# Performance work log

Hardware: AMD Instinct MI355X
Metric: run time of the kernel (lower is better)

The kernel has to match this reference:

```python
import jax, jax.numpy as jnp
import numpy as np

S = 8192          # sequence length
E = 1024          # embedding_dim
H = 2048          # hidden_dim
V = 50257         # vocab_size
T = 50            # tagset_size


def setup_inputs() -> dict:
    key = jax.random.key(0)
    ks = jax.random.split(key, 5)
    scale = 0.02
    return {
        "sentence": jax.random.randint(ks[0], (S,), 0, V),
        "emb": jax.random.normal(ks[1], (V, E), jnp.float32) * scale,
        "W_ih": jax.random.normal(ks[2], (H, E), jnp.float32) * scale,
        "W_hh": jax.random.normal(ks[3], (H, H), jnp.float32) * scale,
        "b_ih": jnp.zeros((H,), jnp.float32),
        "b_hh": jnp.zeros((H,), jnp.float32),
        "W_out": jax.random.normal(ks[4], (T, H), jnp.float32) * scale,
        "b_out": jnp.zeros((T,), jnp.float32),
        "h0": jnp.zeros((H,), jnp.float32),
    }


def reference(sentence, emb, W_ih, W_hh, b_ih, b_hh, W_out, b_out, h0):
    # Embedding lookup: [S, E]
    x = emb[sentence]
    # Precompute input contribution for all timesteps (parallel GEMM): [S, H]
    xi = x @ W_ih.T + b_ih + b_hh

    # Elman recurrence: h_t = tanh(W_ih x_t + b_ih + W_hh h_{t-1} + b_hh)
    def step(h, xi_t):
        h_new = jnp.tanh(xi_t + W_hh @ h)
        return h_new, h_new

    _, rnn_out = jax.lax.scan(step, h0, xi)  # rnn_out: [S, H]

    # Linear head + log_softmax over tags
    tag_space = rnn_out @ W_out.T + b_out    # [S, T]
    return jax.nn.log_softmax(tag_space, axis=-1)
```

## Files before the change

kernel.cpp:

```cpp
#include <hip/hip_runtime.h>
#include <hip/hip_bf16.h>

#define S_LEN 8192
#define E_DIM 1024
#define H_DIM 2048
#define T_TAGS 50
#define NWG 256
#define RPW (H_DIM / NWG)

typedef short short8 __attribute__((ext_vector_type(8)));
typedef float floatx4 __attribute__((ext_vector_type(4)));
typedef _Float16 half8 __attribute__((ext_vector_type(8)));
typedef _Float16 half2v __attribute__((ext_vector_type(2)));
typedef unsigned int uint4a __attribute__((ext_vector_type(4)));

__device__ __forceinline__ unsigned short f2bf(float f) {
    unsigned u = __builtin_bit_cast(unsigned, f);
    unsigned r = (u + 0x7fffu + ((u >> 16) & 1u)) >> 16;
    return (unsigned short)r;
}

__device__ __forceinline__ float dot8(half8 a, half8 b, float acc) {
#if __has_builtin(__builtin_amdgcn_fdot2)
    union U { half8 v; half2v p[4]; };
    U ua; ua.v = a; U ub; ub.v = b;
    acc = __builtin_amdgcn_fdot2(ua.p[0], ub.p[0], acc, false);
    acc = __builtin_amdgcn_fdot2(ua.p[1], ub.p[1], acc, false);
    acc = __builtin_amdgcn_fdot2(ua.p[2], ub.p[2], acc, false);
    acc = __builtin_amdgcn_fdot2(ua.p[3], ub.p[3], acc, false);
#else
    #pragma unroll
    for (int i = 0; i < 8; ++i) acc += (float)a[i] * (float)b[i];
#endif
    return acc;
}

__device__ __forceinline__ float fast_tanh(float x) {
    float xc = fminf(fmaxf(x, -9.f), 9.f);
    float e = __expf(2.f * xc);
    return (e - 1.f) / (e + 1.f);
}

#define TAGOK(A, B)                                                          \
    (((A.x >> 16) == tg) & ((A.y >> 16) == tg) & ((A.z >> 16) == tg) &       \
     ((A.w >> 16) == tg) & ((B.x >> 16) == tg) & ((B.y >> 16) == tg) &       \
     ((B.z >> 16) == tg) & ((B.w >> 16) == tg))

__global__ __launch_bounds__(256) void cast_kernel(
        const float* __restrict__ whh, const float* __restrict__ wih,
        const float* __restrict__ wout,
        _Float16* __restrict__ whh_h, unsigned short* __restrict__ wih_b,
        _Float16* __restrict__ wout_h) {
    const int nWhh = H_DIM * H_DIM;
    const int nWih = H_DIM * E_DIM;
    const int nWout = 64 * H_DIM;
    long long i = (long long)blockIdx.x * 256 + threadIdx.x;
    if (i < nWhh) { whh_h[i] = (_Float16)whh[i]; return; }
    i -= nWhh;
    if (i < nWih) { wih_b[i] = f2bf(wih[i]); return; }
    i -= nWih;
    if (i < nWout) {
        int r = (int)(i >> 11), c = (int)(i & 2047);
        wout_h[i] = (r < T_TAGS) ? (_Float16)wout[r * H_DIM + c] : (_Float16)0.f;
    }
}

__global__ __launch_bounds__(256) void embed_kernel(
        const int* __restrict__ sent, const float* __restrict__ emb,
        unsigned short* __restrict__ Xb) {
    size_t i = (size_t)blockIdx.x * 256 + threadIdx.x;
    size_t s = i >> 10, e = i & 1023;
    Xb[i] = f2bf(emb[(size_t)sent[s] * E_DIM + e]);
}

__global__ __launch_bounds__(256) void xi_gemm(
        const unsigned short* __restrict__ Xb, const unsigned short* __restrict__ Wb,
        const float* __restrict__ bih, const float* __restrict__ bhh,
        float* __restrict__ xi) {
    int lane = threadIdx.x & 63;
    int w = threadIdx.x >> 6;
    int m0 = blockIdx.y * 64 + w * 16;
    int n0 = blockIdx.x * 16;
    int mi = m0 + (lane & 15);
    int ni = n0 + (lane & 15);
    int q8 = (lane >> 4) * 8;
    const short8* arow = (const short8*)(Xb + (size_t)mi * E_DIM + q8);
    const short8* brow = (const short8*)(Wb + (size_t)ni * E_DIM + q8);
    floatx4 acc = {0.f, 0.f, 0.f, 0.f};
    #pragma unroll 4
    for (int k = 0; k < E_DIM / 32; ++k) {
        short8 a = arow[k * 4];
        short8 b = brow[k * 4];
        acc = __builtin_amdgcn_mfma_f32_16x16x32_bf16(a, b, acc, 0, 0, 0);
    }
    float bias = bih[ni] + bhh[ni];
    int rbase = (lane >> 4) * 4;
    #pragma unroll
    for (int i = 0; i < 4; ++i) {
        xi[(size_t)(m0 + rbase + i) * H_DIM + ni] = acc[i] + bias;
    }
}

__global__ __launch_bounds__(256) void init_hpk(
        const float* __restrict__ h0, unsigned* __restrict__ hpk,
        unsigned* __restrict__ hx) {
    int i = blockIdx.x * 256 + threadIdx.x;
    if (i < H_DIM) {
        unsigned short hb = __builtin_bit_cast(unsigned short, (_Float16)h0[i]);
        unsigned pk = (unsigned)hb;
        hpk[i] = pk;
        hpk[H_DIM + i] = 0xFFFF0000u;
        #pragma unroll
        for (int x = 0; x < 8; ++x) {
            hx[(size_t)x * 2 * H_DIM + i] = pk;
            hx[(size_t)x * 2 * H_DIM + H_DIM + i] = 0xFFFF0000u;
        }
    }
}

__global__ __launch_bounds__(256, 1) void rnn_seq(
        const _Float16* __restrict__ Whh, const float* __restrict__ xi,
        unsigned* __restrict__ hpk, unsigned* __restrict__ hx,
        unsigned* __restrict__ ctl, _Float16* __restrict__ rnn) {
    __shared__ __align__(16) _Float16 hlds[2][H_DIM];
    __shared__ float xilds[2][64];
    __shared__ int sh_xcd, sh_rank, sh_fast;
    const int tid = threadIdx.x;
    const int wg = blockIdx.x;

    if (tid == 0) {
        unsigned x;
        asm volatile("s_getreg_b32 %0, hwreg(HW_REG_XCC_ID)" : "=s"(x));
        x &= 7u;
        unsigned rk = __hip_atomic_fetch_add(&ctl[x], 1u, __ATOMIC_RELAXED,
                                             __HIP_MEMORY_SCOPE_AGENT);
        __hip_atomic_fetch_add(&ctl[8], 1u, __ATOMIC_RELEASE,
                               __HIP_MEMORY_SCOPE_AGENT);
        while (__hip_atomic_load(&ctl[8], __ATOMIC_ACQUIRE,
                                 __HIP_MEMORY_SCOPE_AGENT) < (unsigned)NWG)
            __builtin_amdgcn_s_sleep(2);
        int fast = 1;
        for (int k = 0; k < 8; ++k)
            fast &= (__hip_atomic_load(&ctl[k], __ATOMIC_RELAXED,
                                       __HIP_MEMORY_SCOPE_AGENT) == 32u);
        sh_xcd = (int)x; sh_rank = (int)rk; sh_fast = fast;
    }
    __syncthreads();
    const int xcd = sh_xcd, rank = sh_rank, use_fast = sh_fast;

    if (use_fast && rank < 32) {
        const int lane = tid & 63;
        const int wv = tid >> 6;
        const int wgrow = rank * 64;
        unsigned* hxl = hx + (size_t)xcd * 2 * H_DIM;

        half8 w[16][4];
        {
            const _Float16* wb = Whh + (size_t)(wgrow + wv * 16) * H_DIM + lane * 8;
            #pragma unroll
            for (int i = 0; i < 16; ++i) {
                const half8* rp = (const half8*)(wb + (size_t)i * H_DIM);
                asm volatile(
                    "global_load_dwordx4 %0, %4, off\n\t"
                    "global_load_dwordx4 %1, %5, off\n\t"
                    "global_load_dwordx4 %2, %6, off\n\t"
                    "global_load_dwordx4 %3, %7, off\n\t"
                    "s_waitcnt vmcnt(0)"
                    : "=&v"(w[i][0]), "=&v"(w[i][1]), "=&v"(w[i][2]), "=&v"(w[i][3])
                    : "v"(rp), "v"(rp + 64), "v"(rp + 128), "v"(rp + 192));
            }
        }
        if (tid < 64) xilds[0][tid] = xi[wgrow + tid];
        __syncthreads();

        const int lr = ((lane & 1) << 3) | (((lane >> 1) & 1) << 2) |
                       (((lane >> 2) & 1) << 1) | ((lane >> 3) & 1);

        for (int t = 0; t < S_LEN; ++t) {
            float xnext = 0.f;
            if (tid < 64 && t + 1 < S_LEN)
                xnext = xi[(size_t)(t + 1) * H_DIM + wgrow + tid];

            const uint4a* p = (const uint4a*)(hxl + (size_t)(t & 1) * H_DIM) + tid * 2;
            const unsigned tg = (unsigned)t;
            uint4a a, b;
            int rounds = 0;
            for (;;) {
                if (rounds < 24) {
                    asm volatile(
                        "global_load_dwordx4 %0, %2, off sc0 nt\n\t"
                        "global_load_dwordx4 %1, %3, off sc0 nt\n\t"
                        "s_waitcnt vmcnt(0)"
                        : "=&v"(a), "=&v"(b) : "v"(p), "v"(p + 1) : "memory");
                } else {
                    asm volatile(
                        "global_load_dwordx4 %0, %2, off sc0 sc1\n\t"
                        "global_load_dwordx4 %1, %3, off sc0 sc1\n\t"
                        "s_waitcnt vmcnt(0)"
                        : "=&v"(a), "=&v"(b) : "v"(p), "v"(p + 1) : "memory");
                }
                bool ok = TAGOK(a, b);
                if (ok) break;
                ++rounds;
                if (rounds > 2) __builtin_amdgcn_s_sleep(1);
            }
            uint4a hp;
            hp.x = (a.x & 0xffffu) | (a.y << 16);
            hp.y = (a.z & 0xffffu) | (a.w << 16);
            hp.z = (b.x & 0xffffu) | (b.y << 16);
            hp.w = (b.z & 0xffffu) | (b.w << 16);
            *(uint4a*)&hlds[t & 1][tid * 8] = hp;
            if (tid < 64) xilds[(t + 1) & 1][tid] = xnext;
            __syncthreads();

            half8 hv[4];
            {
                const half8* hb = (const half8*)&hlds[t & 1][lane * 8];
                #pragma unroll
                for (int j = 0; j < 4; ++j) hv[j] = hb[j * 64];
            }
            float acc[16];
            #pragma unroll
            for (int i = 0; i < 16; ++i) {
                float s = 0.f;
                #pragma unroll
                for (int j = 0; j < 4; ++j) s = dot8(w[i][j], hv[j], s);
                acc[i] = s;
            }

            {
                bool hi = lane & 1;
                #pragma unroll
                for (int i = 0; i < 8; ++i) {
                    float snd = hi ? acc[i] : acc[i + 8];
                    float kp  = hi ? acc[i + 8] : acc[i];
                    acc[i] = kp + __shfl_xor(snd, 1);
                }
                hi = lane & 2;
                #pragma unroll
                for (int i = 0; i < 4; ++i) {
                    float snd = hi ? acc[i] : acc[i + 4];
                    float kp  = hi ? acc[i + 4] : acc[i];
                    acc[i] = kp + __shfl_xor(snd, 2);
                }
                hi = lane & 4;
                #pragma unroll
                for (int i = 0; i < 2; ++i) {
                    float snd = hi ? acc[i] : acc[i + 2];
                    float kp  = hi ? acc[i + 2] : acc[i];
                    acc[i] = kp + __shfl_xor(snd, 4);
                }
                hi = lane & 8;
                {
                    float snd = hi ? acc[0] : acc[1];
                    float kp  = hi ? acc[1] : acc[0];
                    acc[0] = kp + __shfl_xor(snd, 8);
                }
                acc[0] += __shfl_xor(acc[0], 16);
                acc[0] += __shfl_xor(acc[0], 32);
            }

            if (lane < 16) {
                int lrow = wv * 16 + lr;
                float hvf = fast_tanh(xilds[t & 1][lrow] + acc[0]);
                _Float16 hf = (_Float16)hvf;
                unsigned pk = ((unsigned)(t + 1) << 16)
                            | (unsigned)__builtin_bit_cast(unsigned short, hf);
                unsigned* dst = hxl + (size_t)((t + 1) & 1) * H_DIM + wgrow + lrow;
                asm volatile("global_store_dword %0, %1, off sc0 sc1"
                             :: "v"(dst), "v"(pk) : "memory");
                if (xcd == 0)
                    rnn[(size_t)t * H_DIM + wgrow + lrow] = hf;
            }
        }
    } else {
        const int rowbase = wg * RPW;
        const int r = tid >> 5;
        const int j = tid & 31;
        half8 wreg[8];
        {
            const half8* wrow = (const half8*)(Whh + (size_t)(rowbase + r) * H_DIM);
            #pragma unroll
            for (int c = 0; c < 8; ++c) wreg[c] = wrow[j + c * 32];
        }
        if (tid < RPW) xilds[0][tid] = xi[rowbase + tid];
        __syncthreads();

        for (int t = 0; t < S_LEN; ++t) {
            float xnext = 0.f;
            if (tid < RPW && t + 1 < S_LEN)
                xnext = xi[(size_t)(t + 1) * H_DIM + rowbase + tid];

            const uint4a* p0 = (const uint4a*)(hpk + (size_t)(t & 1) * H_DIM) + tid * 2;
            const unsigned tg = (unsigned)t;
            uint4a a = {}, b = {};
            bool got0 = false, got1 = false;
            int round = 0;
            for (;;) {
                if (!got0)
                    asm volatile("global_load_dwordx4 %0, %1, off sc0 sc1"
                                 : "=v"(a) : "v"(p0) : "memory");
                if (!got1)
                    asm volatile("global_load_dwordx4 %0, %1, off sc0 sc1"
                                 : "=v"(b) : "v"(p0 + 1) : "memory");
                asm volatile("s_waitcnt vmcnt(0)" ::: "memory");
                got0 = got0 | (((a.x >> 16) == tg) & ((a.y >> 16) == tg) &
                               ((a.z >> 16) == tg) & ((a.w >> 16) == tg));
                got1 = got1 | (((b.x >> 16) == tg) & ((b.y >> 16) == tg) &
                               ((b.z >> 16) == tg) & ((b.w >> 16) == tg));
                if (got0 && got1) break;
                if (++round > 1) __builtin_amdgcn_s_sleep(1);
            }
            uint4a hp;
            hp.x = (a.x & 0xffffu) | (a.y << 16);
            hp.y = (a.z & 0xffffu) | (a.w << 16);
            hp.z = (b.x & 0xffffu) | (b.y << 16);
            hp.w = (b.z & 0xffffu) | (b.w << 16);
            *(uint4a*)&hlds[t & 1][tid * 8] = hp;
            if (tid < RPW) xilds[(t + 1) & 1][tid] = xnext;
            __syncthreads();

            float acc = 0.f;
            const _Float16* hpt = &hlds[t & 1][j * 8];
            #pragma unroll
            for (int c = 0; c < 8; ++c) {
                half8 hvv = *(const half8*)(hpt + c * 256);
                acc = dot8(wreg[c], hvv, acc);
            }
            acc += __shfl_xor(acc, 1);  acc += __shfl_xor(acc, 2);
            acc += __shfl_xor(acc, 4);  acc += __shfl_xor(acc, 8);
            acc += __shfl_xor(acc, 16);

            if (j == 0) {
                float hvf = fast_tanh(xilds[t & 1][r] + acc);
                _Float16 hf = (_Float16)hvf;
                unsigned pk = ((unsigned)(t + 1) << 16)
                            | (unsigned)__builtin_bit_cast(unsigned short, hf);
                __hip_atomic_store(&hpk[(size_t)((t + 1) & 1) * H_DIM + rowbase + r], pk,
                                   __ATOMIC_RELAXED, __HIP_MEMORY_SCOPE_AGENT);
                rnn[(size_t)t * H_DIM + rowbase + r] = hf;
            }
        }
    }
}

__global__ __launch_bounds__(256) void head_kernel(
        const _Float16* __restrict__ rnn, const _Float16* __restrict__ Wout,
        const float* __restrict__ bout, float* __restrict__ out) {
    __shared__ __align__(16) _Float16 h8[8][H_DIM];
    __shared__ __align__(16) _Float16 wr[H_DIM];
    __shared__ float tl[8][T_TAGS];
    int tid = threadIdx.x;
    size_t sbase = (size_t)blockIdx.x * 8;
    {
        const uint4* src = (const uint4*)(rnn + sbase * H_DIM);
        uint4* dst = (uint4*)&h8[0][0];
        for (int i = tid; i < 8 * H_DIM / 8; i += 256) dst[i] = src[i];
    }
    __syncthreads();
    int sl = ((tid >> 6) << 1) | ((tid >> 5) & 1);
    int l32 = tid & 31;
    for (int t = 0; t < T_TAGS; ++t) {
        ((uint4*)wr)[tid] = ((const uint4*)(Wout + t * H_DIM))[tid];
        __syncthreads();
        float acc = 0.f;
        const _Float16* hp = &h8[sl][l32 * 64];
        const _Float16* wp = &wr[l32 * 64];
        #pragma unroll
        for (int c = 0; c < 8; ++c)
            acc = dot8(*(const half8*)(hp + c * 8), *(const half8*)(wp + c * 8), acc);
        acc += __shfl_xor(acc, 1);  acc += __shfl_xor(acc, 2);
        acc += __shfl_xor(acc, 4);  acc += __shfl_xor(acc, 8);
        acc += __shfl_xor(acc, 16);
        if (l32 == 0) tl[sl][t] = acc + bout[t];
        __syncthreads();
    }
    if (tid < 8) {
        float m = -1e30f;
        for (int t = 0; t < T_TAGS; ++t) m = fmaxf(m, tl[tid][t]);
        float sum = 0.f;
        for (int t = 0; t < T_TAGS; ++t) sum += expf(tl[tid][t] - m);
        float lse = m + logf(sum);
        for (int t = 0; t < T_TAGS; ++t) out[(sbase + tid) * T_TAGS + t] = tl[tid][t] - lse;
    }
}

extern "C" void kernel_launch(void* const* d_in, const int* in_sizes, int n_in,
                              void* d_out, int out_size, void* d_ws, size_t ws_size,
                              hipStream_t stream) {
    const int*   sent = (const int*)  d_in[0];
    const float* emb  = (const float*)d_in[1];
    const float* wih  = (const float*)d_in[2];
    const float* whh  = (const float*)d_in[3];
    const float* bih  = (const float*)d_in[4];
    const float* bhh  = (const float*)d_in[5];
    const float* wout = (const float*)d_in[6];
    const float* bout = (const float*)d_in[7];
    const float* h0   = (const float*)d_in[8];

    char* ws = (char*)d_ws;
    _Float16*       whh_h  = (_Float16*)      (ws + 0);
    unsigned short* wih_b  = (unsigned short*)(ws + 8388608);
    _Float16*       wout_h = (_Float16*)      (ws + 12582912);
    unsigned short* X_b    = (unsigned short*)(ws + 12845056);
    unsigned*       hx     = (unsigned*)      (ws + 13000704);
    unsigned*       hpk    = (unsigned*)      (ws + 29605888);
    float*          xi     = (float*)         (ws + 29622272);
    _Float16*       rnn    = (_Float16*)      (ws + 96731136);
    unsigned*       ctl    = (unsigned*)      (ws + 130285568);

    hipMemsetAsync(ctl, 0, 64, stream);
    {
        const int total = H_DIM * H_DIM + H_DIM * E_DIM + 64 * H_DIM;
        cast_kernel<<<(total + 255) / 256, 256, 0, stream>>>(
            whh, wih, wout, whh_h, wih_b, wout_h);
    }
    embed_kernel<<<(S_LEN * E_DIM) / 256, 256, 0, stream>>>(sent, emb, X_b);
    xi_gemm<<<dim3(H_DIM / 16, S_LEN / 64), 256, 0, stream>>>(X_b, wih_b, bih, bhh, xi);
    init_hpk<<<H_DIM / 256, 256, 0, stream>>>(h0, hpk, hx);
    rnn_seq<<<NWG, 256, 0, stream>>>(whh_h, xi, hpk, hx, ctl, rnn);
    head_kernel<<<S_LEN / 8, 256, 0, stream>>>(rnn, wout_h, bout, (float*)d_out);
}
```

Baseline: 27.10 ms.

## Double RNN workgroup size to 512 threads, halving rows per wave

Launches the recurrent kernel with 512 threads per workgroup, so each of the 8 waves holds 8 rows of W_hh in registers instead of 16. Each thread then polls and unpacks one 16-byte chunk of the hidden-state exchange buffer instead of two. The shuffle reduction tree is shortened to match. The aim is to cut per-step serial latency: less dot-product work per wave, and more waves to hide the polling and LDS latency. The fallback path gates its work to the first 256 threads. The cost is a wider __syncthreads barrier, and launch_bounds(512,2) may limit registers, which risks spilling the weight array.

```diff
diff --git a/kernel.cpp b/kernel.cpp
--- a/kernel.cpp
+++ b/kernel.cpp
@@ -118,7 +118,7 @@
     }
 }
 
-__global__ __launch_bounds__(256, 1) void rnn_seq(
+__global__ __launch_bounds__(512, 2) void rnn_seq(
         const _Float16* __restrict__ Whh, const float* __restrict__ xi,
         unsigned* __restrict__ hpk, unsigned* __restrict__ hx,
         unsigned* __restrict__ ctl, _Float16* __restrict__ rnn) {
@@ -154,11 +154,11 @@
         const int wgrow = rank * 64;
         unsigned* hxl = hx + (size_t)xcd * 2 * H_DIM;
 
-        half8 w[16][4];
+        half8 w[8][4];
         {
-            const _Float16* wb = Whh + (size_t)(wgrow + wv * 16) * H_DIM + lane * 8;
+            const _Float16* wb = Whh + (size_t)(wgrow + wv * 8) * H_DIM + lane * 8;
             #pragma unroll
-            for (int i = 0; i < 16; ++i) {
+            for (int i = 0; i < 8; ++i) {
                 const half8* rp = (const half8*)(wb + (size_t)i * H_DIM);
                 asm volatile(
                     "global_load_dwordx4 %0, %4, off\n\t"
@@ -173,43 +173,42 @@
         if (tid < 64) xilds[0][tid] = xi[wgrow + tid];
         __syncthreads();
 
-        const int lr = ((lane & 1) << 3) | (((lane >> 1) & 1) << 2) |
-                       (((lane >> 2) & 1) << 1) | ((lane >> 3) & 1);
+        const int lr3 = ((lane & 1) << 2) | (lane & 2) | ((lane >> 2) & 1);
+        const int lrow = wv * 8 + lr3;
 
         for (int t = 0; t < S_LEN; ++t) {
             float xnext = 0.f;
             if (tid < 64 && t + 1 < S_LEN)
                 xnext = xi[(size_t)(t + 1) * H_DIM + wgrow + tid];
 
-            const uint4a* p = (const uint4a*)(hxl + (size_t)(t & 1) * H_DIM) + tid * 2;
+            const uint4a* p = (const uint4a*)(hxl + (size_t)(t & 1) * H_DIM) + tid;
             const unsigned tg = (unsigned)t;
-            uint4a a, b;
+            uint4a a;
             int rounds = 0;
             for (;;) {
                 if (rounds < 24) {
                     asm volatile(
-                        "global_load_dwordx4 %0, %2, off sc0 nt\n\t"
-                        "global_load_dwordx4 %1, %3, off sc0 nt\n\t"
+                        "global_load_dwordx4 %0, %1, off sc0 nt\n\t"
                         "s_waitcnt vmcnt(0)"
-                        : "=&v"(a), "=&v"(b) : "v"(p), "v"(p + 1) : "memory");
+                        : "=&v"(a) : "v"(p) : "memory");
                 } else {
                     asm volatile(
-                        "global_load_dwordx4 %0, %2, off sc0 sc1\n\t"
-                        "global_load_dwordx4 %1, %3, off sc0 sc1\n\t"
+                        "global_load_dwordx4 %0, %1, off sc0 sc1\n\t"
                         "s_waitcnt vmcnt(0)"
-                        : "=&v"(a), "=&v"(b) : "v"(p), "v"(p + 1) : "memory");
-                }
-                bool ok = TAGOK(a, b);
+                        : "=&v"(a) : "v"(p) : "memory");
+                }
+                bool ok = ((a.x >> 16) == tg) & ((a.y >> 16) == tg) &
+                          ((a.z >> 16) == tg) & ((a.w >> 16) == tg);
                 if (ok) break;
                 ++rounds;
                 if (rounds > 2) __builtin_amdgcn_s_sleep(1);
             }
-            uint4a hp;
-            hp.x = (a.x & 0xffffu) | (a.y << 16);
-            hp.y = (a.z & 0xffffu) | (a.w << 16);
-            hp.z = (b.x & 0xffffu) | (b.y << 16);
-            hp.w = (b.z & 0xffffu) | (b.w << 16);
-            *(uint4a*)&hlds[t & 1][tid * 8] = hp;
+            {
+                uint2 hp2;
+                hp2.x = (a.x & 0xffffu) | (a.y << 16);
+                hp2.y = (a.z & 0xffffu) | (a.w << 16);
+                *(uint2*)&hlds[t & 1][tid * 4] = hp2;
+            }
             if (tid < 64) xilds[(t + 1) & 1][tid] = xnext;
             __syncthreads();
 
@@ -219,9 +218,9 @@
                 #pragma unroll
                 for (int j = 0; j < 4; ++j) hv[j] = hb[j * 64];
             }
-            float acc[16];
+            float acc[8];
             #pragma unroll
-            for (int i = 0; i < 16; ++i) {
+            for (int i = 0; i < 8; ++i) {
                 float s = 0.f;
                 #pragma unroll
                 for (int j = 0; j < 4; ++j) s = dot8(w[i][j], hv[j], s);
@@ -231,37 +230,30 @@
             {
                 bool hi = lane & 1;
                 #pragma unroll
-                for (int i = 0; i < 8; ++i) {
-                    float snd = hi ? acc[i] : acc[i + 8];
-                    float kp  = hi ? acc[i + 8] : acc[i];
-                    acc[i] = kp + __shfl_xor(snd, 1);
-                }
-                hi = lane & 2;
-                #pragma unroll
                 for (int i = 0; i < 4; ++i) {
                     float snd = hi ? acc[i] : acc[i + 4];
                     float kp  = hi ? acc[i + 4] : acc[i];
-                    acc[i] = kp + __shfl_xor(snd, 2);
-                }
-                hi = lane & 4;
+                    acc[i] = kp + __shfl_xor(snd, 1);
+                }
+                hi = lane & 2;
                 #pragma unroll
                 for (int i = 0; i < 2; ++i) {
                     float snd = hi ? acc[i] : acc[i + 2];
                     float kp  = hi ? acc[i + 2] : acc[i];
-                    acc[i] = kp + __shfl_xor(snd, 4);
-                }
-                hi = lane & 8;
+                    acc[i] = kp + __shfl_xor(snd, 2);
+                }
+                hi = lane & 4;
                 {
                     float snd = hi ? acc[0] : acc[1];
                     float kp  = hi ? acc[1] : acc[0];
-                    acc[0] = kp + __shfl_xor(snd, 8);
-                }
+                    acc[0] = kp + __shfl_xor(snd, 4);
+                }
+                acc[0] += __shfl_xor(acc[0], 8);
                 acc[0] += __shfl_xor(acc[0], 16);
                 acc[0] += __shfl_xor(acc[0], 32);
             }
 
-            if (lane < 16) {
-                int lrow = wv * 16 + lr;
+            if (lane < 8) {
                 float hvf = fast_tanh(xilds[t & 1][lrow] + acc[0]);
                 _Float16 hf = (_Float16)hvf;
                 unsigned pk = ((unsigned)(t + 1) << 16)
@@ -275,10 +267,10 @@
         }
     } else {
         const int rowbase = wg * RPW;
-        const int r = tid >> 5;
+        const int r = (tid & 255) >> 5;
         const int j = tid & 31;
         half8 wreg[8];
-        {
+        if (tid < 256) {
             const half8* wrow = (const half8*)(Whh + (size_t)(rowbase + r) * H_DIM);
             #pragma unroll
             for (int c = 0; c < 8; ++c) wreg[c] = wrow[j + c * 32];
@@ -291,54 +283,58 @@
             if (tid < RPW && t + 1 < S_LEN)
                 xnext = xi[(size_t)(t + 1) * H_DIM + rowbase + tid];
 
-            const uint4a* p0 = (const uint4a*)(hpk + (size_t)(t & 1) * H_DIM) + tid * 2;
-            const unsigned tg = (unsigned)t;
-            uint4a a = {}, b = {};
-            bool got0 = false, got1 = false;
-            int round = 0;
-            for (;;) {
-                if (!got0)
-                    asm volatile("global_load_dwordx4 %0, %1, off sc0 sc1"
-                                 : "=v"(a) : "v"(p0) : "memory");
-                if (!got1)
-                    asm volatile("global_load_dwordx4 %0, %1, off sc0 sc1"
-                                 : "=v"(b) : "v"(p0 + 1) : "memory");
-                asm volatile("s_waitcnt vmcnt(0)" ::: "memory");
-                got0 = got0 | (((a.x >> 16) == tg) & ((a.y >> 16) == tg) &
-                               ((a.z >> 16) == tg) & ((a.w >> 16) == tg));
-                got1 = got1 | (((b.x >> 16) == tg) & ((b.y >> 16) == tg) &
-                               ((b.z >> 16) == tg) & ((b.w >> 16) == tg));
-                if (got0 && got1) break;
-                if (++round > 1) __builtin_amdgcn_s_sleep(1);
-            }
-            uint4a hp;
-            hp.x = (a.x & 0xffffu) | (a.y << 16);
-            hp.y = (a.z & 0xffffu) | (a.w << 16);
-            hp.z = (b.x & 0xffffu) | (b.y << 16);
-            hp.w = (b.z & 0xffffu) | (b.w << 16);
-            *(uint4a*)&hlds[t & 1][tid * 8] = hp;
+            if (tid < 256) {
+                const uint4a* p0 = (const uint4a*)(hpk + (size_t)(t & 1) * H_DIM) + tid * 2;
+                const unsigned tg = (unsigned)t;
+                uint4a a = {}, b = {};
+                bool got0 = false, got1 = false;
+                int round = 0;
+                for (;;) {
+                    if (!got0)
+                        asm volatile("global_load_dwordx4 %0, %1, off sc0 sc1"
+                                     : "=v"(a) : "v"(p0) : "memory");
+                    if (!got1)
+                        asm volatile("global_load_dwordx4 %0, %1, off sc0 sc1"
+                                     : "=v"(b) : "v"(p0 + 1) : "memory");
+                    asm volatile("s_waitcnt vmcnt(0)" ::: "memory");
+                    got0 = got0 | (((a.x >> 16) == tg) & ((a.y >> 16) == tg) &
+                                   ((a.z >> 16) == tg) & ((a.w >> 16) == tg));
+                    got1 = got1 | (((b.x >> 16) == tg) & ((b.y >> 16) == tg) &
+                                   ((b.z >> 16) == tg) & ((b.w >> 16) == tg));
+                    if (got0 && got1) break;
+                    if (++round > 1) __builtin_amdgcn_s_sleep(1);
+                }
+                uint4a hp;
+                hp.x = (a.x & 0xffffu) | (a.y << 16);
+                hp.y = (a.z & 0xffffu) | (a.w << 16);
+                hp.z = (b.x & 0xffffu) | (b.y << 16);
+                hp.w = (b.z & 0xffffu) | (b.w << 16);
+                *(uint4a*)&hlds[t & 1][tid * 8] = hp;
+            }
             if (tid < RPW) xilds[(t + 1) & 1][tid] = xnext;
             __syncthreads();
 
-            float acc = 0.f;
-            const _Float16* hpt = &hlds[t & 1][j * 8];
-            #pragma unroll
-            for (int c = 0; c < 8; ++c) {
-                half8 hvv = *(const half8*)(hpt + c * 256);
-                acc = dot8(wreg[c], hvv, acc);
-            }
-            acc += __shfl_xor(acc, 1);  acc += __shfl_xor(acc, 2);
-            acc += __shfl_xor(acc, 4);  acc += __shfl_xor(acc, 8);
-            acc += __shfl_xor(acc, 16);
-
-            if (j == 0) {
-                float hvf = fast_tanh(xilds[t & 1][r] + acc);
-                _Float16 hf = (_Float16)hvf;
-                unsigned pk = ((unsigned)(t + 1) << 16)
-                            | (unsigned)__builtin_bit_cast(unsigned short, hf);
-                __hip_atomic_store(&hpk[(size_t)((t + 1) & 1) * H_DIM + rowbase + r], pk,
-                                   __ATOMIC_RELAXED, __HIP_MEMORY_SCOPE_AGENT);
-                rnn[(size_t)t * H_DIM + rowbase + r] = hf;
+            if (tid < 256) {
+                float acc = 0.f;
+                const _Float16* hpt = &hlds[t & 1][j * 8];
+                #pragma unroll
+                for (int c = 0; c < 8; ++c) {
+                    half8 hvv = *(const half8*)(hpt + c * 256);
+                    acc = dot8(wreg[c], hvv, acc);
+                }
+                acc += __shfl_xor(acc, 1);  acc += __shfl_xor(acc, 2);
+                acc += __shfl_xor(acc, 4);  acc += __shfl_xor(acc, 8);
+                acc += __shfl_xor(acc, 16);
+
+                if (j == 0) {
+                    float hvf = fast_tanh(xilds[t & 1][r] + acc);
+                    _Float16 hf = (_Float16)hvf;
+                    unsigned pk = ((unsigned)(t + 1) << 16)
+                                | (unsigned)__builtin_bit_cast(unsigned short, hf);
+                    __hip_atomic_store(&hpk[(size_t)((t + 1) & 1) * H_DIM + rowbase + r], pk,
+                                       __ATOMIC_RELAXED, __HIP_MEMORY_SCOPE_AGENT);
+                    rnn[(size_t)t * H_DIM + rowbase + r] = hf;
+                }
             }
         }
     }
@@ -418,6 +414,6 @@
     embed_kernel<<<(S_LEN * E_DIM) / 256, 256, 0, stream>>>(sent, emb, X_b);
     xi_gemm<<<dim3(H_DIM / 16, S_LEN / 64), 256, 0, stream>>>(X_b, wih_b, bih, bhh, xi);
     init_hpk<<<H_DIM / 256, 256, 0, stream>>>(h0, hpk, hx);
-    rnn_seq<<<NWG, 256, 0, stream>>>(whh_h, xi, hpk, hx, ctl, rnn);
+    rnn_seq<<<NWG, 512, 0, stream>>>(whh_h, xi, hpk, hx, ctl, rnn);
     head_kernel<<<S_LEN / 8, 256, 0, stream>>>(rnn, wout_h, bout, (float*)d_out);
 }
```

After: 25.32 ms. 6.6% less time.
